# Performance work log

Hardware: AMD Instinct MI355X
Metric: run time of the kernel (lower is better)

The kernel has to match this reference:

```python
import jax, jax.numpy as jnp
import numpy as np

HIDDEN_NF = 128
NORMALIZATION_FACTOR = 100.0


def setup_inputs() -> dict:
    key = jax.random.key(0)
    ks = jax.random.split(key, 10)
    N, E, H, D_EDGE = 50000, 800000, HIDDEN_NF, 1
    in_dim = 2 * H + D_EDGE  # 257
    h = jax.random.normal(ks[0], (N, H), dtype=jnp.float32)
    coord = jax.random.normal(ks[1], (N, 3), dtype=jnp.float32)
    edge_index = jax.random.randint(ks[2], (2, E), 0, N, dtype=jnp.int32)
    coord_diff = jax.random.normal(ks[3], (E, 3), dtype=jnp.float32)
    edge_attr = jax.random.normal(ks[4], (E, D_EDGE), dtype=jnp.float32)
    node_mask = jnp.ones((N, 1), dtype=jnp.float32)
    edge_mask = jnp.ones((E, 1), dtype=jnp.float32)
    # coord_mlp params: Dense(H) -> silu -> Dense(H) -> silu -> Dense(1, no bias)
    def glorot(k, fan_in, fan_out):
        lim = np.sqrt(6.0 / (fan_in + fan_out))
        return jax.random.uniform(k, (fan_in, fan_out), jnp.float32, -lim, lim)
    W1 = glorot(ks[5], in_dim, H)
    b1 = jnp.zeros((H,), jnp.float32)
    W2 = glorot(ks[6], H, H)
    b2 = jnp.zeros((H,), jnp.float32)
    # final layer: variance_scaling(0.001**2, fan_avg, uniform)
    lim3 = np.sqrt(3.0 * (0.001 ** 2) / ((H + 1) / 2.0))
    W3 = jax.random.uniform(ks[7], (H, 1), jnp.float32, -lim3, lim3)
    return {"h": h, "coord": coord, "edge_index": edge_index,
            "coord_diff": coord_diff, "edge_attr": edge_attr,
            "node_mask": node_mask, "edge_mask": edge_mask,
            "W1": W1, "b1": b1, "W2": W2, "b2": b2, "W3": W3}


def reference(h, coord, edge_index, coord_diff, edge_attr, node_mask, edge_mask,
              W1, b1, W2, b2, W3):
    row, col = edge_index[0], edge_index[1]
    # [E, 2H+1] gather + concat
    inp = jnp.concatenate([h[row], h[col], edge_attr], axis=1)
    x = jax.nn.silu(inp @ W1 + b1)
    x = jax.nn.silu(x @ W2 + b2)
    scale = x @ W3                       # [E, 1]
    trans = coord_diff * scale           # [E, 3]
    trans = trans * edge_mask
    agg = jax.ops.segment_sum(trans, row, num_segments=coord.shape[0])
    agg = agg / NORMALIZATION_FACTOR     # aggregation_method == 'sum'
    coord = coord + agg
    coord = coord * node_mask
    return coord
```

## Files before the change

### kernel.cpp

```cpp
#include <hip/hip_runtime.h>
#include <hip/hip_bf16.h>

typedef __attribute__((ext_vector_type(8))) short short8;
typedef __attribute__((ext_vector_type(4))) float f32x4;
typedef __attribute__((ext_vector_type(2))) float f32x2;
typedef unsigned short u16;
typedef unsigned int u32;
typedef unsigned char u8;
typedef unsigned long long u64;
typedef long long i64;

#define NORM_INV (1.0f / 100.0f)

__device__ __forceinline__ float silu(float x) {
    return x * __builtin_amdgcn_rcpf(1.0f + __expf(-x));
}

__device__ __forceinline__ u16 f2bf(float x) {
    union { float f; u32 u; } v; v.f = x;
    u32 r = v.u + 0x7fff + ((v.u >> 16) & 1);
    return (u16)(r >> 16);
}

__global__ void prep_weights(const float* __restrict__ W1, const float* __restrict__ W2,
                             u16* __restrict__ W1abT, u8* __restrict__ W2T8) {
    int idx = blockIdx.x * blockDim.x + threadIdx.x;
    if (idx < 256 * 128) {
        int j = idx >> 7, k = idx & 127;
        float v = (j < 128) ? W1[k * 128 + j] : W1[(128 + k) * 128 + (j - 128)];
        W1abT[j * 128 + k] = f2bf(v);
    } else if (idx < 256 * 128 + 128 * 128) {
        int t = idx - 256 * 128;
        int n = t >> 7, k = t & 127;
        float v = W2[k * 128 + n];
        int pk = __builtin_amdgcn_cvt_pk_fp8_f32(v, v, 0, false);
        W2T8[n * 128 + k] = (u8)pk;
    }
}

__global__ __launch_bounds__(256) void ab_kernel(const float* __restrict__ h,
        const float* __restrict__ b1, const u16* __restrict__ W1abT,
        u8* __restrict__ AB8, int N) {
    __shared__ u16 hs[32 * 128];
    int tid = threadIdx.x;
    int n0 = blockIdx.x * 32;
    int lane = tid & 63, wave = tid >> 6;

    #pragma unroll
    for (int it = 0; it < 8; ++it) {
        int item = it * 256 + tid;
        int m = item >> 6;
        int k = (item & 63) * 2;
        float2 hv = make_float2(0.f, 0.f);
        if (n0 + m < N) hv = *(const float2*)(h + (size_t)(n0 + m) * 128 + k);
        u32 pk = (u32)f2bf(hv.x) | ((u32)f2bf(hv.y) << 16);
        int byteoff = m * 256 + ((k * 2) ^ ((m & 7) << 4));
        *(u32*)((char*)hs + byteoff) = pk;
    }

    short8 bw[4][4];
    #pragma unroll
    for (int nt = 0; nt < 4; ++nt) {
        int j = wave * 64 + nt * 16 + (lane & 15);
        #pragma unroll
        for (int ks = 0; ks < 4; ++ks)
            bw[nt][ks] = *(const short8*)((const char*)W1abT + j * 256 + ks * 64 + (lane >> 4) * 16);
    }
    __syncthreads();

    f32x4 acc[2][4] = {};
    #pragma unroll
    for (int ks = 0; ks < 4; ++ks) {
        short8 a[2];
        #pragma unroll
        for (int mt = 0; mt < 2; ++mt) {
            int row = mt * 16 + (lane & 15);
            int byteoff = row * 256 + (((ks * 64) + ((lane >> 4) * 16)) ^ ((row & 7) << 4));
            a[mt] = *(short8*)((char*)hs + byteoff);
        }
        #pragma unroll
        for (int mt = 0; mt < 2; ++mt)
            #pragma unroll
            for (int nt = 0; nt < 4; ++nt)
                acc[mt][nt] = __builtin_amdgcn_mfma_f32_16x16x32_bf16(a[mt], bw[nt][ks], acc[mt][nt], 0, 0, 0);
    }

    #pragma unroll
    for (int mt = 0; mt < 2; ++mt) {
        #pragma unroll
        for (int nt = 0; nt < 4; ++nt) {
            int j = wave * 64 + nt * 16 + (lane & 15);
            float bias = (j < 128) ? b1[j] : 0.f;
            #pragma unroll
            for (int r = 0; r < 4; ++r) {
                int node = n0 + mt * 16 + (lane >> 4) * 4 + r;
                if (node < N) {
                    float v = acc[mt][nt][r] + bias;
                    int pk = __builtin_amdgcn_cvt_pk_fp8_f32(v, v, 0, false);
                    AB8[(size_t)node * 256 + j] = (u8)pk;
                }
            }
        }
    }
}

__device__ __forceinline__ i64 conv_frag(uint2 va, uint2 vb, float eac, float4 w0, float4 w1) {
    f32x2 fa[4], fb[4];
    fa[0] = __builtin_amdgcn_cvt_pk_f32_fp8(va.x, false);
    fa[1] = __builtin_amdgcn_cvt_pk_f32_fp8(va.x, true);
    fa[2] = __builtin_amdgcn_cvt_pk_f32_fp8(va.y, false);
    fa[3] = __builtin_amdgcn_cvt_pk_f32_fp8(va.y, true);
    fb[0] = __builtin_amdgcn_cvt_pk_f32_fp8(vb.x, false);
    fb[1] = __builtin_amdgcn_cvt_pk_f32_fp8(vb.x, true);
    fb[2] = __builtin_amdgcn_cvt_pk_f32_fp8(vb.y, false);
    fb[3] = __builtin_amdgcn_cvt_pk_f32_fp8(vb.y, true);
    const float wc[8] = { w0.x, w0.y, w0.z, w0.w, w1.x, w1.y, w1.z, w1.w };
    float x[8];
    #pragma unroll
    for (int jp = 0; jp < 4; ++jp) {
        x[2 * jp]     = silu(fa[jp].x + fb[jp].x + eac * wc[2 * jp]);
        x[2 * jp + 1] = silu(fa[jp].y + fb[jp].y + eac * wc[2 * jp + 1]);
    }
    u32 lo = 0, hi = 0;
    lo = __builtin_amdgcn_cvt_pk_fp8_f32(x[0], x[1], lo, false);
    lo = __builtin_amdgcn_cvt_pk_fp8_f32(x[2], x[3], lo, true);
    hi = __builtin_amdgcn_cvt_pk_fp8_f32(x[4], x[5], hi, false);
    hi = __builtin_amdgcn_cvt_pk_fp8_f32(x[6], x[7], hi, true);
    union { uint2 u; i64 l; } c; c.u = make_uint2(lo, hi);
    return c.l;
}

__global__ __launch_bounds__(256) void edge_kernel(
        const u8* __restrict__ AB8, const u8* __restrict__ W2T8,
        const int* __restrict__ eidx, const float* __restrict__ coord_diff,
        const float* __restrict__ edge_attr, const float* __restrict__ edge_mask,
        const float* __restrict__ W1, const float* __restrict__ b2,
        const float* __restrict__ W3, float* __restrict__ agg, int E) {
    __shared__ u8 w2s8[128 * 128];
    __shared__ float ssc[4][16];
    __shared__ float sw1c[128];
    __shared__ float2 sb2w3[128];

    const int tid = threadIdx.x;
    const int lane = tid & 63;
    const int wv = tid >> 6;
    const int le = lane & 15;
    const int lg = lane >> 4;

    #pragma unroll
    for (int it = 0; it < 8; ++it) {
        int idx = it * 256 + tid;
        int row = idx >> 4, c8 = idx & 15;
        u64 v = *(const u64*)(W2T8 + row * 128 + c8 * 8);
        *(u64*)(w2s8 + row * 128 + ((c8 * 8) ^ ((row & 7) << 4))) = v;
    }
    if (tid < 128) {
        sw1c[tid] = W1[256 * 128 + tid];
        sb2w3[tid] = make_float2(b2[tid], W3[tid]);
    }
    __syncthreads();

    const int ntiles = (E + 15) >> 4;
    const int wpb = blockDim.x >> 6;
    const int nwaves = gridDim.x * wpb;
    int tile = blockIdx.x * wpb + wv;
    if (tile >= ntiles) return;

    int e0 = tile << 4;
    int ep = min(e0 + le, E - 1);
    int rowc = eidx[ep];
    int colc = eidx[E + ep];
    float eac = edge_attr[ep];

    while (true) {
        uint2 va[4], vb[4];
        {
            const char* rp = (const char*)(AB8 + (size_t)rowc * 256);
            const char* cp = (const char*)(AB8 + (size_t)colc * 256 + 128);
            #pragma unroll
            for (int ks = 0; ks < 4; ++ks) {
                va[ks] = *(const uint2*)(rp + ks * 32 + lg * 8);
                vb[ks] = *(const uint2*)(cp + ks * 32 + lg * 8);
            }
        }
        float eml = edge_mask[min(e0 + le, E - 1)];
        float cdl = coord_diff[min(e0 * 3 + lane, E * 3 - 1)];

        int next = tile + nwaves;
        bool hn = next < ntiles;
        int ne0 = (hn ? next : tile) << 4;
        int nep = min(ne0 + le, E - 1);
        int rown = eidx[nep];
        int coln = eidx[E + nep];
        float ean = edge_attr[nep];

        int z0 = 0;
        asm volatile("" : "+v"(z0));
        float4 wq[8];
        #pragma unroll
        for (int ks = 0; ks < 4; ++ks) {
            wq[2 * ks]     = *(const float4*)&sw1c[z0 + ks * 32 + lg * 8];
            wq[2 * ks + 1] = *(const float4*)&sw1c[z0 + ks * 32 + lg * 8 + 4];
        }

        i64 pa[4];
        #pragma unroll
        for (int ks = 0; ks < 4; ++ks)
            pa[ks] = conv_frag(va[ks], vb[ks], eac, wq[2 * ks], wq[2 * ks + 1]);

        int z1 = 0;
        asm volatile("" : "+v"(z1));
        float s[4] = { 0.f, 0.f, 0.f, 0.f };
        #pragma unroll
        for (int hf = 0; hf < 2; ++hf) {
            f32x4 acc[4] = {};
            #pragma unroll
            for (int ks = 0; ks < 4; ++ks) {
                #pragma unroll
                for (int nt = 0; nt < 4; ++nt) {
                    int row = (hf * 4 + nt) * 16 + le;
                    u64 b8 = *(const u64*)(w2s8 + row * 128 +
                             (((ks * 32) + (lg * 8)) ^ ((le & 7) << 4)));
                    acc[nt] = __builtin_amdgcn_mfma_f32_16x16x32_fp8_fp8(pa[ks], (i64)b8, acc[nt], 0, 0, 0);
                }
            }
            float2 bw[4];
            #pragma unroll
            for (int nt = 0; nt < 4; ++nt)
                bw[nt] = sb2w3[z1 + (hf * 4 + nt) * 16 + le];
            #pragma unroll
            for (int nt = 0; nt < 4; ++nt) {
                #pragma unroll
                for (int r = 0; r < 4; ++r)
                    s[r] += silu(acc[nt][r] + bw[nt].x) * bw[nt].y;
            }
        }
        #pragma unroll
        for (int r = 0; r < 4; ++r) {
            float t = s[r];
            t += __shfl_xor(t, 1);
            t += __shfl_xor(t, 2);
            t += __shfl_xor(t, 4);
            t += __shfl_xor(t, 8);
            s[r] = t;
        }
        if (le == 0) {
            f32x4 sv = { s[0], s[1], s[2], s[3] };
            *(f32x4*)&ssc[wv][lg * 4] = sv;
        }

        int els = (lane < 48) ? (lane / 3) : 0;
        int rA = __shfl(rowc, els);
        float emA = __shfl(eml, els);
        float sc = ssc[wv][els];
        if (lane < 48 && (e0 + els) < E)
            atomicAdd(&agg[rA * 3 + (lane - els * 3)], cdl * emA * sc);

        if (!hn) break;
        tile = next; e0 = ne0;
        rowc = rown; colc = coln; eac = ean;
    }
}

__global__ void finalize(const float* __restrict__ coord, const float* __restrict__ agg,
                         const float* __restrict__ node_mask, float* __restrict__ out, int n3) {
    int i = blockIdx.x * blockDim.x + threadIdx.x;
    if (i < n3) {
        int n = i / 3;
        out[i] = (coord[i] + agg[i] * NORM_INV) * node_mask[n];
    }
}

extern "C" void kernel_launch(void* const* d_in, const int* in_sizes, int n_in,
                              void* d_out, int out_size, void* d_ws, size_t ws_size,
                              hipStream_t stream) {
    const float* h          = (const float*)d_in[0];
    const float* coord      = (const float*)d_in[1];
    const int*   eidx       = (const int*)d_in[2];
    const float* coord_diff = (const float*)d_in[3];
    const float* edge_attr  = (const float*)d_in[4];
    const float* node_mask  = (const float*)d_in[5];
    const float* edge_mask  = (const float*)d_in[6];
    const float* W1         = (const float*)d_in[7];
    const float* b1         = (const float*)d_in[8];
    const float* W2         = (const float*)d_in[9];
    const float* b2         = (const float*)d_in[10];
    const float* W3         = (const float*)d_in[11];

    int N = in_sizes[0] / 128;
    int E = in_sizes[2] / 2;

    char* ws = (char*)d_ws;
    size_t off = 0;
    u8*  AB8   = (u8*)(ws + off);  off += (size_t)N * 256; off = (off + 255) & ~(size_t)255;
    u16* W1abT = (u16*)(ws + off); off += 256 * 128 * sizeof(u16);
    u8*  W2T8  = (u8*)(ws + off);  off += 128 * 128; off = (off + 255) & ~(size_t)255;
    float* agg = (float*)(ws + off); off += (size_t)N * 3 * sizeof(float);

    hipMemsetAsync(agg, 0, (size_t)N * 3 * sizeof(float), stream);
    hipLaunchKernelGGL(prep_weights, dim3(192), dim3(256), 0, stream, W1, W2, W1abT, W2T8);
    hipLaunchKernelGGL(ab_kernel, dim3((N + 31) / 32), dim3(256), 0, stream, h, b1, W1abT, AB8, N);
    hipLaunchKernelGGL(edge_kernel, dim3(2048), dim3(256), 0, stream,
                       AB8, W2T8, eidx, coord_diff, edge_attr, edge_mask, W1, b2, W3, agg, E);
    int n3 = N * 3;
    hipLaunchKernelGGL(finalize, dim3((n3 + 255) / 256), dim3(256), 0, stream,
                       coord, agg, node_mask, (float*)d_out, n3);
}
```

Before: 117.6 us.

## Hold W2 fragments in registers instead of LDS and vectorize elementwise math

Each lane now loads its 32 W2 fp8 fragments straight from global memory into registers once per wave, instead of staging a swizzled 16 KB copy in LDS and rereading it on every tile. This removes the LDS traffic and the block-level staging before the MFMA loop. The elementwise math is also rewritten with packed f32x2/f32x4 vector ops, which may let the compiler emit packed FMA instructions. The cost is 64 extra VGPRs per lane, which could lower occupancy or cause spills. LDS use per block also drops sharply.

New measurement: 145.7 us. 1.24x slower.

```diff
diff --git a/kernel.cpp b/kernel.cpp
--- a/kernel.cpp
+++ b/kernel.cpp
@@ -104,39 +104,12 @@
     }
 }
 
-__device__ __forceinline__ i64 conv_frag(uint2 va, uint2 vb, float eac, float4 w0, float4 w1) {
-    f32x2 fa[4], fb[4];
-    fa[0] = __builtin_amdgcn_cvt_pk_f32_fp8(va.x, false);
-    fa[1] = __builtin_amdgcn_cvt_pk_f32_fp8(va.x, true);
-    fa[2] = __builtin_amdgcn_cvt_pk_f32_fp8(va.y, false);
-    fa[3] = __builtin_amdgcn_cvt_pk_f32_fp8(va.y, true);
-    fb[0] = __builtin_amdgcn_cvt_pk_f32_fp8(vb.x, false);
-    fb[1] = __builtin_amdgcn_cvt_pk_f32_fp8(vb.x, true);
-    fb[2] = __builtin_amdgcn_cvt_pk_f32_fp8(vb.y, false);
-    fb[3] = __builtin_amdgcn_cvt_pk_f32_fp8(vb.y, true);
-    const float wc[8] = { w0.x, w0.y, w0.z, w0.w, w1.x, w1.y, w1.z, w1.w };
-    float x[8];
-    #pragma unroll
-    for (int jp = 0; jp < 4; ++jp) {
-        x[2 * jp]     = silu(fa[jp].x + fb[jp].x + eac * wc[2 * jp]);
-        x[2 * jp + 1] = silu(fa[jp].y + fb[jp].y + eac * wc[2 * jp + 1]);
-    }
-    u32 lo = 0, hi = 0;
-    lo = __builtin_amdgcn_cvt_pk_fp8_f32(x[0], x[1], lo, false);
-    lo = __builtin_amdgcn_cvt_pk_fp8_f32(x[2], x[3], lo, true);
-    hi = __builtin_amdgcn_cvt_pk_fp8_f32(x[4], x[5], hi, false);
-    hi = __builtin_amdgcn_cvt_pk_fp8_f32(x[6], x[7], hi, true);
-    union { uint2 u; i64 l; } c; c.u = make_uint2(lo, hi);
-    return c.l;
-}
-
 __global__ __launch_bounds__(256) void edge_kernel(
         const u8* __restrict__ AB8, const u8* __restrict__ W2T8,
         const int* __restrict__ eidx, const float* __restrict__ coord_diff,
         const float* __restrict__ edge_attr, const float* __restrict__ edge_mask,
         const float* __restrict__ W1, const float* __restrict__ b2,
         const float* __restrict__ W3, float* __restrict__ agg, int E) {
-    __shared__ u8 w2s8[128 * 128];
     __shared__ float ssc[4][16];
     __shared__ float sw1c[128];
     __shared__ float2 sb2w3[128];
@@ -147,18 +120,22 @@
     const int le = lane & 15;
     const int lg = lane >> 4;
 
-    #pragma unroll
-    for (int it = 0; it < 8; ++it) {
-        int idx = it * 256 + tid;
-        int row = idx >> 4, c8 = idx & 15;
-        u64 v = *(const u64*)(W2T8 + row * 128 + c8 * 8);
-        *(u64*)(w2s8 + row * 128 + ((c8 * 8) ^ ((row & 7) << 4))) = v;
-    }
     if (tid < 128) {
         sw1c[tid] = W1[256 * 128 + tid];
         sb2w3[tid] = make_float2(b2[tid], W3[tid]);
     }
     __syncthreads();
+
+    i64 bw[2][4][4];
+    #pragma unroll
+    for (int hf = 0; hf < 2; ++hf)
+        #pragma unroll
+        for (int ks = 0; ks < 4; ++ks)
+            #pragma unroll
+            for (int nt = 0; nt < 4; ++nt) {
+                int row = (hf * 4 + nt) * 16 + le;
+                bw[hf][ks][nt] = *(const i64*)(W2T8 + row * 128 + ks * 32 + lg * 8);
+            }
 
     const int ntiles = (E + 15) >> 4;
     const int wpb = blockDim.x >> 6;
@@ -196,57 +173,72 @@
 
         int z0 = 0;
         asm volatile("" : "+v"(z0));
-        float4 wq[8];
+        const f32x2 eacv = { eac, eac };
+        i64 pa[4];
         #pragma unroll
         for (int ks = 0; ks < 4; ++ks) {
-            wq[2 * ks]     = *(const float4*)&sw1c[z0 + ks * 32 + lg * 8];
-            wq[2 * ks + 1] = *(const float4*)&sw1c[z0 + ks * 32 + lg * 8 + 4];
-        }
-
-        i64 pa[4];
-        #pragma unroll
-        for (int ks = 0; ks < 4; ++ks)
-            pa[ks] = conv_frag(va[ks], vb[ks], eac, wq[2 * ks], wq[2 * ks + 1]);
+            f32x2 wc[4];
+            #pragma unroll
+            for (int jp = 0; jp < 4; ++jp)
+                wc[jp] = *(const f32x2*)&sw1c[z0 + ks * 32 + lg * 8 + 2 * jp];
+            f32x2 fa[4], fb[4];
+            fa[0] = __builtin_amdgcn_cvt_pk_f32_fp8(va[ks].x, false);
+            fa[1] = __builtin_amdgcn_cvt_pk_f32_fp8(va[ks].x, true);
+            fa[2] = __builtin_amdgcn_cvt_pk_f32_fp8(va[ks].y, false);
+            fa[3] = __builtin_amdgcn_cvt_pk_f32_fp8(va[ks].y, true);
+            fb[0] = __builtin_amdgcn_cvt_pk_f32_fp8(vb[ks].x, false);
+            fb[1] = __builtin_amdgcn_cvt_pk_f32_fp8(vb[ks].x, true);
+            fb[2] = __builtin_amdgcn_cvt_pk_f32_fp8(vb[ks].y, false);
+            fb[3] = __builtin_amdgcn_cvt_pk_f32_fp8(vb[ks].y, true);
+            float x[8];
+            #pragma unroll
+            for (int jp = 0; jp < 4; ++jp) {
+                f32x2 pre = (fa[jp] + fb[jp]) + eacv * wc[jp];
+                x[2 * jp]     = silu(pre.x);
+                x[2 * jp + 1] = silu(pre.y);
+            }
+            u32 lo = 0, hi = 0;
+            lo = __builtin_amdgcn_cvt_pk_fp8_f32(x[0], x[1], lo, false);
+            lo = __builtin_amdgcn_cvt_pk_fp8_f32(x[2], x[3], lo, true);
+            hi = __builtin_amdgcn_cvt_pk_fp8_f32(x[4], x[5], hi, false);
+            hi = __builtin_amdgcn_cvt_pk_fp8_f32(x[6], x[7], hi, true);
+            union { uint2 u; i64 l; } c; c.u = make_uint2(lo, hi);
+            pa[ks] = c.l;
+        }
 
         int z1 = 0;
         asm volatile("" : "+v"(z1));
-        float s[4] = { 0.f, 0.f, 0.f, 0.f };
+        f32x4 sv = { 0.f, 0.f, 0.f, 0.f };
         #pragma unroll
         for (int hf = 0; hf < 2; ++hf) {
             f32x4 acc[4] = {};
             #pragma unroll
-            for (int ks = 0; ks < 4; ++ks) {
+            for (int ks = 0; ks < 4; ++ks)
                 #pragma unroll
-                for (int nt = 0; nt < 4; ++nt) {
-                    int row = (hf * 4 + nt) * 16 + le;
-                    u64 b8 = *(const u64*)(w2s8 + row * 128 +
-                             (((ks * 32) + (lg * 8)) ^ ((le & 7) << 4)));
-                    acc[nt] = __builtin_amdgcn_mfma_f32_16x16x32_fp8_fp8(pa[ks], (i64)b8, acc[nt], 0, 0, 0);
-                }
-            }
-            float2 bw[4];
-            #pragma unroll
-            for (int nt = 0; nt < 4; ++nt)
-                bw[nt] = sb2w3[z1 + (hf * 4 + nt) * 16 + le];
+                for (int nt = 0; nt < 4; ++nt)
+                    acc[nt] = __builtin_amdgcn_mfma_f32_16x16x32_fp8_fp8(pa[ks], bw[hf][ks][nt], acc[nt], 0, 0, 0);
             #pragma unroll
             for (int nt = 0; nt < 4; ++nt) {
-                #pragma unroll
-                for (int r = 0; r < 4; ++r)
-                    s[r] += silu(acc[nt][r] + bw[nt].x) * bw[nt].y;
+                float2 bwv = sb2w3[z1 + (hf * 4 + nt) * 16 + le];
+                f32x4 b2v = { bwv.x, bwv.x, bwv.x, bwv.x };
+                f32x4 w3v = { bwv.y, bwv.y, bwv.y, bwv.y };
+                f32x4 v = acc[nt] + b2v;
+                f32x4 y = { silu(v.x), silu(v.y), silu(v.z), silu(v.w) };
+                sv = sv + y * w3v;
             }
         }
         #pragma unroll
         for (int r = 0; r < 4; ++r) {
-            float t = s[r];
+            float t = sv[r];
             t += __shfl_xor(t, 1);
             t += __shfl_xor(t, 2);
             t += __shfl_xor(t, 4);
             t += __shfl_xor(t, 8);
-            s[r] = t;
+            sv[r] = t;
         }
         if (le == 0) {
-            f32x4 sv = { s[0], s[1], s[2], s[3] };
-            *(f32x4*)&ssc[wv][lg * 4] = sv;
+            f32x4 o = { sv.x, sv.y, sv.z, sv.w };
+            *(f32x4*)&ssc[wv][lg * 4] = o;
         }
 
         int els = (lane < 48) ? (lane / 3) : 0;
```
